# Kernel optimization log

Hardware: AMD Instinct MI355X
Metric: run time of the kernel (lower is better)

Reference implementation:

```python
import jax, jax.numpy as jnp
import numpy as np

K, D_IN, D_OUT, R = 64, 256, 256, 64
TOK_PER_E = 4096
N_TOK = K * TOK_PER_E


def setup_inputs() -> dict:
    key = jax.random.key(0)
    k1, k2, k3, k4 = jax.random.split(key, 4)
    inp = jax.random.normal(k1, (N_TOK, D_IN), jnp.float32)
    # kaiming-uniform-ish scale for expert weights
    weight = jax.random.normal(k2, (K, D_OUT, D_IN), jnp.float32) * (1.0 / np.sqrt(D_IN))
    bias = jax.random.normal(k3, (K, D_OUT), jnp.float32) * 0.02
    # c_psuedo_inv built exactly as in __init__ from components [k, d, r]
    components = jax.random.normal(k4, (K, D_OUT, R), jnp.float32)
    gram = jnp.einsum('kdr,kds->krs', components, components)          # [k, r, r]
    c_inv = jnp.linalg.inv(gram)
    c_psuedo_inv = jnp.einsum('kdr,krs,kds->kds', components, c_inv, components)  # [k, d, d]
    fwd_expert_count = jnp.full((K,), TOK_PER_E, dtype=jnp.int32)
    return {
        'inp': inp,
        'fwd_expert_count': fwd_expert_count,
        'weight': weight,
        'bias': bias,
        'c_psuedo_inv': c_psuedo_inv,
        'max_tokens': TOK_PER_E,
    }


def reference(inp, fwd_expert_count, weight, bias, c_psuedo_inv, max_tokens):
    counts = fwd_expert_count                      # [k]
    k = counts.shape[0]
    n = inp.shape[0]
    offsets = jnp.concatenate([jnp.zeros((1,), counts.dtype), jnp.cumsum(counts)])  # [k+1]
    expert_ids = jnp.repeat(jnp.arange(k, dtype=counts.dtype), counts,
                            total_repeat_length=n)                                   # [n]
    token_pos = jnp.arange(n, dtype=counts.dtype) - offsets[expert_ids]              # [n]

    # Scatter ragged tokens into padded [k, max_tokens, in_feat], then do the
    # grouped linear as one batched GEMM (padded rows are zero; masked after bias).
    padded_in = jnp.zeros((k, max_tokens, inp.shape[1]), inp.dtype)
    padded_in = padded_in.at[expert_ids, token_pos].set(inp)
    x_pad = jnp.einsum('ktd,ked->kte', padded_in, weight) + bias[:, None, :]         # [k, t, e]
    valid = (jnp.arange(max_tokens)[None, :] < counts[:, None])[..., None]
    x_pad = jnp.where(valid, x_pad, jnp.zeros((), x_pad.dtype))

    padded = jnp.transpose(x_pad, (1, 0, 2))                                         # [t, k, e]
    return jnp.einsum('nkd,kds->nks', padded, c_psuedo_inv)                          # [t, k, e]
```

## Files before the change

kernel.cpp:

```cpp
#include <hip/hip_runtime.h>
#include <hip/hip_bf16.h>
#include <stdint.h>


typedef unsigned int   u32;
typedef unsigned short u16;

typedef short bf16x8 __attribute__((ext_vector_type(8)));
typedef float f32x4  __attribute__((ext_vector_type(4)));

__device__ __forceinline__ bf16x8 pack8(const float* v) {
  union { __hip_bfloat16 h[8]; bf16x8 v8; } r;
#pragma unroll
  for (int j = 0; j < 8; ++j) r.h[j] = __float2bfloat16(v[j]);
  return r.v8;
}
__device__ __forceinline__ u16 f2bf1(float f) {
  union { __hip_bfloat16 h; u16 u; } r;
  r.h = __float2bfloat16(f);
  return r.u;
}
__device__ __forceinline__ u32 pk2(float a, float b) {
  union { __hip_bfloat162 h; u32 u; } r;
  r.h.x = __float2bfloat16(a);
  r.h.y = __float2bfloat16(b);
  return r.u;
}
__device__ __forceinline__ void gload_lds16(const void* g, void* l) {
  __builtin_amdgcn_global_load_lds((__attribute__((address_space(1))) void*)g,
                                   (__attribute__((address_space(3))) void*)l,
                                   16, 0, 0);
}

__global__ __launch_bounds__(256, 2) void k_m(const float* __restrict__ P,
                                              const float* __restrict__ W,
                                              const float* __restrict__ bias,
                                              u16* __restrict__ Mt,
                                              float* __restrict__ b2) {
  const int k = blockIdx.y;
  const int tid = threadIdx.x;
  __shared__ __align__(16) unsigned char LDS[65536];
  const float* Pk = P + (size_t)k * 16384;

  if (blockIdx.x == 4) {
    const int sq = tid & 15, ec = tid >> 4;
    const float* bk = bias + k * 256;
    f32x4 acc = {};
#pragma unroll
    for (int i = 0; i < 16; ++i) {
      const int e = ec * 16 + i;
      const float4 pv = *reinterpret_cast<const float4*>(Pk + (size_t)e * 64 + sq * 4);
      const float bv = bk[e];
      acc[0] = fmaf(bv, pv.x, acc[0]);
      acc[1] = fmaf(bv, pv.y, acc[1]);
      acc[2] = fmaf(bv, pv.z, acc[2]);
      acc[3] = fmaf(bv, pv.w, acc[3]);
    }
    float* red = reinterpret_cast<float*>(LDS);
    *reinterpret_cast<f32x4*>(red + ec * 64 + sq * 4) = acc;
    __syncthreads();
    if (tid < 64) {
      float sum = 0.f;
#pragma unroll
      for (int c = 0; c < 16; ++c) sum += red[c * 64 + tid];
      b2[k * 64 + tid] = sum;
    }
    return;
  }

  const int d0 = blockIdx.x * 64;
  u32* WT = reinterpret_cast<u32*>(LDS);
  u32* PT = reinterpret_cast<u32*>(LDS + 32768);
  const float* Wk = W + (size_t)k * 65536;
  const int lane = tid & 63, w = tid >> 6, q = lane & 15, g = lane >> 4;

#pragma unroll
  for (int r = 0; r < 8; ++r) {
    const int ep = r * 16 + w * 4 + g;
    const float4 w0 = *reinterpret_cast<const float4*>(Wk + (size_t)(2 * ep) * 256 + d0 + 4 * q);
    const float4 w1 = *reinterpret_cast<const float4*>(Wk + (size_t)(2 * ep + 1) * 256 + d0 + 4 * q);
    const float4 p0 = *reinterpret_cast<const float4*>(Pk + (size_t)(2 * ep) * 64 + 4 * q);
    const float4 p1 = *reinterpret_cast<const float4*>(Pk + (size_t)(2 * ep + 1) * 64 + 4 * q);
    const int c = ep >> 2, cw = ep & 3;
    const float wa[4] = {w0.x, w0.y, w0.z, w0.w};
    const float wb[4] = {w1.x, w1.y, w1.z, w1.w};
    const float pa[4] = {p0.x, p0.y, p0.z, p0.w};
    const float pb[4] = {p1.x, p1.y, p1.z, p1.w};
#pragma unroll
    for (int j = 0; j < 4; ++j) {
      const int rw = 4 * q + j;
      const int sc = c ^ (rw & 7);
      WT[rw * 128 + sc * 4 + cw] = pk2(wa[j], wb[j]);
      PT[rw * 128 + sc * 4 + cw] = pk2(pa[j], pb[j]);
    }
  }
  __syncthreads();

  f32x4 acc[4] = {};
  const int dl = w * 16 + q;
#pragma unroll
  for (int kk = 0; kk < 8; ++kk) {
    const bf16x8 bfr = *reinterpret_cast<const bf16x8*>(
        reinterpret_cast<const char*>(WT) + dl * 512 + (((kk * 4 + g) ^ (dl & 7)) * 16));
#pragma unroll
    for (int m = 0; m < 4; ++m) {
      const int s = m * 16 + q;
      const bf16x8 afr = *reinterpret_cast<const bf16x8*>(
          reinterpret_cast<const char*>(PT) + s * 512 + (((kk * 4 + g) ^ (s & 7)) * 16));
      acc[m] = __builtin_amdgcn_mfma_f32_16x16x32_bf16(afr, bfr, acc[m], 0, 0, 0);
    }
  }
  u16* Mk = Mt + (size_t)k * 16384;
#pragma unroll
  for (int m = 0; m < 4; ++m)
#pragma unroll
    for (int j = 0; j < 4; ++j) {
      const int s = m * 16 + g * 4 + j;
      Mk[(size_t)s * 256 + d0 + w * 16 + q] = f2bf1(acc[m][j]);
    }
}

__global__ __launch_bounds__(256, 2) void k_main(const float* __restrict__ inp,
                                                 const u16* __restrict__ Mt,
                                                 const float* __restrict__ b2,
                                                 float* __restrict__ out) {
  const int tb = blockIdx.x, k = blockIdx.y;
  const int tid = threadIdx.x, lane = tid & 63, w = tid >> 6;
  const int q = lane & 15, g = lane >> 4;
  __shared__ __align__(16) unsigned char LDS[49152];
  u16* Bl = reinterpret_cast<u16*>(LDS);
  float* Wb = reinterpret_cast<float*>(LDS + 32768 + w * 4096);

  const float* Ak = inp + ((size_t)k * 4096 + (size_t)tb * 64 + w * 16 + q) * 256;
  float4 apre[16];
#pragma unroll
  for (int kk = 0; kk < 8; ++kk) {
    apre[2 * kk]     = *reinterpret_cast<const float4*>(Ak + kk * 32 + g * 8);
    apre[2 * kk + 1] = *reinterpret_cast<const float4*>(Ak + kk * 32 + g * 8 + 4);
  }

  const u16* Mk = Mt + (size_t)k * 16384;
#pragma unroll
  for (int r = 0; r < 8; ++r) {
    const int qq = r * 256 + tid;
    const int s = qq >> 5, u = qq & 31;
    gload_lds16(Mk + (size_t)s * 256 + ((u ^ (s & 7)) * 8),
                (char*)Bl + r * 4096 + w * 1024);
  }
  f32x4 acc[4] = {};
  __syncthreads();

#pragma unroll
  for (int kk = 0; kk < 8; ++kk) {
    bf16x8 mt[4];
#pragma unroll
    for (int n = 0; n < 4; ++n) {
      const int s = n * 16 + q;
      mt[n] = *reinterpret_cast<const bf16x8*>(
          (const char*)Bl + s * 512 + (((kk * 4 + g) ^ (s & 7)) * 16));
    }
    const float va[8] = {apre[2 * kk][0],     apre[2 * kk][1],
                         apre[2 * kk][2],     apre[2 * kk][3],
                         apre[2 * kk + 1][0], apre[2 * kk + 1][1],
                         apre[2 * kk + 1][2], apre[2 * kk + 1][3]};
    const bf16x8 a = pack8(va);
#pragma unroll
    for (int n = 0; n < 4; ++n)
      acc[n] = __builtin_amdgcn_mfma_f32_16x16x32_bf16(mt[n], a, acc[n], 0, 0, 0);
  }

  const float* b2k = b2 + k * 64;
#pragma unroll
  for (int n = 0; n < 4; ++n) {
    const float4 bv = *reinterpret_cast<const float4*>(b2k + n * 16 + g * 4);
    f32x4 r;
    r[0] = acc[n][0] + bv.x;
    r[1] = acc[n][1] + bv.y;
    r[2] = acc[n][2] + bv.z;
    r[3] = acc[n][3] + bv.w;
    const int ch = n * 4 + g;
    *reinterpret_cast<f32x4*>(Wb + q * 64 + ((ch ^ q) * 4)) = r;
  }
#pragma unroll
  for (int j = 0; j < 4; ++j) {
    const int tq = j * 4 + g;
    const f32x4 v = *reinterpret_cast<const f32x4*>(Wb + tq * 64 + ((q ^ tq) * 4));
    const int t = tb * 64 + w * 16 + tq;
    *reinterpret_cast<f32x4*>(out + (size_t)t * 4096 + k * 64 + q * 4) = v;
  }
}

extern "C" void kernel_launch(void* const* d_in, const int* in_sizes, int n_in,
                              void* d_out, int out_size, void* d_ws, size_t ws_size,
                              hipStream_t stream) {
  const float* inp  = (const float*)d_in[0];
  const float* W    = (const float*)d_in[2];
  const float* bias = (const float*)d_in[3];
  const float* P    = (const float*)d_in[4];

  u16*   Mm = (u16*)d_ws;
  float* b2 = (float*)((char*)d_ws + 2097152);
  float* o  = (float*)d_out;

  k_m   <<<dim3(5, 64),  256, 0, stream>>>(P, W, bias, Mm, b2);
  k_main<<<dim3(64, 64), 256, 0, stream>>>(inp, Mm, b2, o);
}
```

Before: 83.49 us.

## Process four token tiles per block with register prefetch and swap grid axes

The main kernel now handles 256 tokens per block in four 64-token iterations. It loads the M matrix into LDS once and prefetches the next tile's activations into registers while the current tile's MFMAs run. The grid shrinks from 64x64 to 64x16 and the x axis becomes the expert, so neighbouring blocks write adjacent expert columns of the output. Launch bounds go up to 3 blocks per SM. The aim is to amortise the LDS fill of M and hide global load latency, at the cost of fewer blocks and higher register pressure from the prefetch.

```diff
diff --git a/kernel.cpp b/kernel.cpp
--- a/kernel.cpp
+++ b/kernel.cpp
@@ -37,12 +37,12 @@
                                               const float* __restrict__ bias,
                                               u16* __restrict__ Mt,
                                               float* __restrict__ b2) {
-  const int k = blockIdx.y;
+  const int k = blockIdx.x;
   const int tid = threadIdx.x;
   __shared__ __align__(16) unsigned char LDS[65536];
   const float* Pk = P + (size_t)k * 16384;
 
-  if (blockIdx.x == 4) {
+  if (blockIdx.y == 4) {
     const int sq = tid & 15, ec = tid >> 4;
     const float* bk = bias + k * 256;
     f32x4 acc = {};
@@ -68,7 +68,7 @@
     return;
   }
 
-  const int d0 = blockIdx.x * 64;
+  const int d0 = blockIdx.y * 64;
   u32* WT = reinterpret_cast<u32*>(LDS);
   u32* PT = reinterpret_cast<u32*>(LDS + 32768);
   const float* Wk = W + (size_t)k * 65536;
@@ -120,23 +120,23 @@
     }
 }
 
-__global__ __launch_bounds__(256, 2) void k_main(const float* __restrict__ inp,
+__global__ __launch_bounds__(256, 3) void k_main(const float* __restrict__ inp,
                                                  const u16* __restrict__ Mt,
                                                  const float* __restrict__ b2,
                                                  float* __restrict__ out) {
-  const int tb = blockIdx.x, k = blockIdx.y;
+  const int k = blockIdx.x, tb = blockIdx.y;
   const int tid = threadIdx.x, lane = tid & 63, w = tid >> 6;
   const int q = lane & 15, g = lane >> 4;
   __shared__ __align__(16) unsigned char LDS[49152];
   u16* Bl = reinterpret_cast<u16*>(LDS);
   float* Wb = reinterpret_cast<float*>(LDS + 32768 + w * 4096);
 
-  const float* Ak = inp + ((size_t)k * 4096 + (size_t)tb * 64 + w * 16 + q) * 256;
+  const float* Abase = inp + ((size_t)k * 4096 + (size_t)tb * 256 + w * 16 + q) * 256;
   float4 apre[16];
 #pragma unroll
   for (int kk = 0; kk < 8; ++kk) {
-    apre[2 * kk]     = *reinterpret_cast<const float4*>(Ak + kk * 32 + g * 8);
-    apre[2 * kk + 1] = *reinterpret_cast<const float4*>(Ak + kk * 32 + g * 8 + 4);
+    apre[2 * kk]     = *reinterpret_cast<const float4*>(Abase + kk * 32 + g * 8);
+    apre[2 * kk + 1] = *reinterpret_cast<const float4*>(Abase + kk * 32 + g * 8 + 4);
   }
 
   const u16* Mk = Mt + (size_t)k * 16384;
@@ -147,46 +147,60 @@
     gload_lds16(Mk + (size_t)s * 256 + ((u ^ (s & 7)) * 8),
                 (char*)Bl + r * 4096 + w * 1024);
   }
-  f32x4 acc[4] = {};
   __syncthreads();
 
-#pragma unroll
-  for (int kk = 0; kk < 8; ++kk) {
-    bf16x8 mt[4];
+  const float* b2k = b2 + k * 64;
+#pragma unroll
+  for (int it = 0; it < 4; ++it) {
+    bf16x8 abf[8];
+#pragma unroll
+    for (int kk = 0; kk < 8; ++kk) {
+      const float va[8] = {apre[2 * kk][0],     apre[2 * kk][1],
+                           apre[2 * kk][2],     apre[2 * kk][3],
+                           apre[2 * kk + 1][0], apre[2 * kk + 1][1],
+                           apre[2 * kk + 1][2], apre[2 * kk + 1][3]};
+      abf[kk] = pack8(va);
+    }
+    if (it < 3) {
+      const float* An = Abase + (size_t)(it + 1) * 64 * 256;
+#pragma unroll
+      for (int kk = 0; kk < 8; ++kk) {
+        apre[2 * kk]     = *reinterpret_cast<const float4*>(An + kk * 32 + g * 8);
+        apre[2 * kk + 1] = *reinterpret_cast<const float4*>(An + kk * 32 + g * 8 + 4);
+      }
+    }
+    f32x4 acc[4] = {};
+#pragma unroll
+    for (int kk = 0; kk < 8; ++kk) {
+      bf16x8 mt[4];
+#pragma unroll
+      for (int n = 0; n < 4; ++n) {
+        const int s = n * 16 + q;
+        mt[n] = *reinterpret_cast<const bf16x8*>(
+            (const char*)Bl + s * 512 + (((kk * 4 + g) ^ (s & 7)) * 16));
+      }
+#pragma unroll
+      for (int n = 0; n < 4; ++n)
+        acc[n] = __builtin_amdgcn_mfma_f32_16x16x32_bf16(mt[n], abf[kk], acc[n], 0, 0, 0);
+    }
 #pragma unroll
     for (int n = 0; n < 4; ++n) {
-      const int s = n * 16 + q;
-      mt[n] = *reinterpret_cast<const bf16x8*>(
-          (const char*)Bl + s * 512 + (((kk * 4 + g) ^ (s & 7)) * 16));
-    }
-    const float va[8] = {apre[2 * kk][0],     apre[2 * kk][1],
-                         apre[2 * kk][2],     apre[2 * kk][3],
-                         apre[2 * kk + 1][0], apre[2 * kk + 1][1],
-                         apre[2 * kk + 1][2], apre[2 * kk + 1][3]};
-    const bf16x8 a = pack8(va);
-#pragma unroll
-    for (int n = 0; n < 4; ++n)
-      acc[n] = __builtin_amdgcn_mfma_f32_16x16x32_bf16(mt[n], a, acc[n], 0, 0, 0);
-  }
-
-  const float* b2k = b2 + k * 64;
-#pragma unroll
-  for (int n = 0; n < 4; ++n) {
-    const float4 bv = *reinterpret_cast<const float4*>(b2k + n * 16 + g * 4);
-    f32x4 r;
-    r[0] = acc[n][0] + bv.x;
-    r[1] = acc[n][1] + bv.y;
-    r[2] = acc[n][2] + bv.z;
-    r[3] = acc[n][3] + bv.w;
-    const int ch = n * 4 + g;
-    *reinterpret_cast<f32x4*>(Wb + q * 64 + ((ch ^ q) * 4)) = r;
-  }
-#pragma unroll
-  for (int j = 0; j < 4; ++j) {
-    const int tq = j * 4 + g;
-    const f32x4 v = *reinterpret_cast<const f32x4*>(Wb + tq * 64 + ((q ^ tq) * 4));
-    const int t = tb * 64 + w * 16 + tq;
-    *reinterpret_cast<f32x4*>(out + (size_t)t * 4096 + k * 64 + q * 4) = v;
+      const float4 bv = *reinterpret_cast<const float4*>(b2k + n * 16 + g * 4);
+      f32x4 r;
+      r[0] = acc[n][0] + bv.x;
+      r[1] = acc[n][1] + bv.y;
+      r[2] = acc[n][2] + bv.z;
+      r[3] = acc[n][3] + bv.w;
+      const int ch = n * 4 + g;
+      *reinterpret_cast<f32x4*>(Wb + q * 64 + ((ch ^ q) * 4)) = r;
+    }
+#pragma unroll
+    for (int j = 0; j < 4; ++j) {
+      const int tq = j * 4 + g;
+      const f32x4 v = *reinterpret_cast<const f32x4*>(Wb + tq * 64 + ((q ^ tq) * 4));
+      const int t = tb * 256 + it * 64 + w * 16 + tq;
+      *reinterpret_cast<f32x4*>(out + (size_t)t * 4096 + k * 64 + q * 4) = v;
+    }
   }
 }
 
@@ -202,6 +216,6 @@
   float* b2 = (float*)((char*)d_ws + 2097152);
   float* o  = (float*)d_out;
 
-  k_m   <<<dim3(5, 64),  256, 0, stream>>>(P, W, bias, Mm, b2);
-  k_main<<<dim3(64, 64), 256, 0, stream>>>(inp, Mm, b2, o);
-}
+  k_m   <<<dim3(64, 5),  256, 0, stream>>>(P, W, bias, Mm, b2);
+  k_main<<<dim3(64, 16), 256, 0, stream>>>(inp, Mm, b2, o);
+}
```

New measurement: 96.36 us. +15.4%, slower.
